# Kernel optimization log

Measured on AMD Instinct MI355X. Metric: run time of the kernel, lower is better.

Reference implementation:

```python
import jax, jax.numpy as jnp
import numpy as np

N = 524288
D_IN = 128


def setup_inputs() -> dict:
    key = jax.random.key(0)
    k_x, k_th, k_fb, k_xi, k_gb = jax.random.split(key, 5)
    X = jax.random.normal(k_x, (N, D_IN), dtype=jnp.float32)
    # f_linear: D_in -> H2 (=N); weight theta is [N, D_in], bias f_bias [N]
    theta = jax.random.normal(k_th, (N, D_IN), dtype=jnp.float32) * 0.02
    f_bias = jax.random.normal(k_fb, (N,), dtype=jnp.float32) * 0.02
    # g_linear: D_in -> H1 (=2); weight xi is [2, D_in], bias g_bias [2]
    xi = jax.random.normal(k_xi, (2, D_IN), dtype=jnp.float32) * 0.02
    g_bias = jax.random.normal(k_gb, (2,), dtype=jnp.float32) * 0.02
    return {"X": X, "theta": theta, "f_bias": f_bias, "xi": xi, "g_bias": g_bias}


def reference(X, theta, f_bias, xi, g_bias):
    # V[i] = relu(g_linear(X[i]))  -> one batched GEMM: [N,2]
    V = jax.nn.relu(X @ xi.T + g_bias)
    # Full W[i,j] = relu(X[i] . theta[j] + f_bias[j]) is masked by the chord
    # mask eye(N) + offsets (i + 2^k - 1) % N for k in {0,1} = offsets {0, 1}.
    # So only the diagonal and first (circulant) super-diagonal survive:
    # w_diag[i] = relu(X[i] . theta[i]       + f_bias[i])
    # w_sup[i]  = relu(X[i] . theta[(i+1)%N] + f_bias[(i+1)%N])
    w_diag = jax.nn.relu(jnp.einsum("nd,nd->n", X, theta) + f_bias)
    theta_next = jnp.roll(theta, -1, axis=0)
    f_bias_next = jnp.roll(f_bias, -1, axis=0)
    w_sup = jax.nn.relu(jnp.einsum("nd,nd->n", X, theta_next) + f_bias_next)
    # V0 = (W * chord_mask) @ V, computed sparsely: [N,2]
    V0 = w_diag[:, None] * V + w_sup[:, None] * jnp.roll(V, -1, axis=0)
    return V0
```

## Files before the change

### kernel.cpp

```cpp
#include <hip/hip_runtime.h>


constexpr int NROWS = 524288;
constexpr int D     = 128;

__device__ __forceinline__ float dot8(const float4& a, const float4& b,
                                      const float4& c, const float4& d) {
    return a.x*c.x + a.y*c.y + a.z*c.z + a.w*c.w
         + b.x*d.x + b.y*d.y + b.z*d.z + b.w*d.w;
}

__global__ __launch_bounds__(256, 4) void smf_kernel(
    const float* __restrict__ X,
    const float* __restrict__ theta,
    const float* __restrict__ f_bias,
    const float* __restrict__ xi,
    const float* __restrict__ g_bias,
    float* __restrict__ out)
{
    const int tid  = blockIdx.x * blockDim.x + threadIdx.x;
    const int wid  = tid >> 6;
    const int lane = threadIdx.x & 63;
    const int grp  = lane >> 4;
    const int q    = lane & 15;
    const int col  = q * 8;

    const int i   = wid * 4 + grp;
    const int ip1 = (i + 1 == NROWS) ? 0 : i + 1;

    const float* xrow  = X     + (size_t)i   * D + col;
    const float* xnrow = X     + (size_t)ip1 * D + col;
    const float* trow  = theta + (size_t)i   * D + col;
    const float* tnrow = theta + (size_t)ip1 * D + col;

    const float4 xa   = *reinterpret_cast<const float4*>(xrow);
    const float4 xb   = *reinterpret_cast<const float4*>(xrow + 4);
    const float4 xna  = *reinterpret_cast<const float4*>(xnrow);
    const float4 xnb  = *reinterpret_cast<const float4*>(xnrow + 4);
    const float4 ta   = *reinterpret_cast<const float4*>(trow);
    const float4 tb   = *reinterpret_cast<const float4*>(trow + 4);
    const float4 tna  = *reinterpret_cast<const float4*>(tnrow);
    const float4 tnb  = *reinterpret_cast<const float4*>(tnrow + 4);
    const float4 xi0a = *reinterpret_cast<const float4*>(xi + col);
    const float4 xi0b = *reinterpret_cast<const float4*>(xi + col + 4);
    const float4 xi1a = *reinterpret_cast<const float4*>(xi + D + col);
    const float4 xi1b = *reinterpret_cast<const float4*>(xi + D + col + 4);

    const float fb  = f_bias[i];
    const float fbn = f_bias[ip1];
    const float gb0 = g_bias[0];
    const float gb1 = g_bias[1];

    float d_diag = dot8(xa, xb, ta, tb);
    float d_sup  = dot8(xa, xb, tna, tnb);
    float vi0    = dot8(xa, xb, xi0a, xi0b);
    float vi1    = dot8(xa, xb, xi1a, xi1b);
    float vn0    = dot8(xna, xnb, xi0a, xi0b);
    float vn1    = dot8(xna, xnb, xi1a, xi1b);

    #pragma unroll
    for (int m = 8; m >= 1; m >>= 1) {
        d_diag += __shfl_xor(d_diag, m, 64);
        d_sup  += __shfl_xor(d_sup,  m, 64);
        vi0    += __shfl_xor(vi0,    m, 64);
        vi1    += __shfl_xor(vi1,    m, 64);
        vn0    += __shfl_xor(vn0,    m, 64);
        vn1    += __shfl_xor(vn1,    m, 64);
    }

    if (q == 0) {
        const float w_diag = fmaxf(d_diag + fb,  0.f);
        const float w_sup  = fmaxf(d_sup  + fbn, 0.f);
        const float v0 = fmaxf(vi0 + gb0, 0.f);
        const float v1 = fmaxf(vi1 + gb1, 0.f);
        const float u0 = fmaxf(vn0 + gb0, 0.f);
        const float u1 = fmaxf(vn1 + gb1, 0.f);
        float2 o;
        o.x = w_diag * v0 + w_sup * u0;
        o.y = w_diag * v1 + w_sup * u1;
        *reinterpret_cast<float2*>(out + (size_t)i * 2) = o;
    }
}

extern "C" void kernel_launch(void* const* d_in, const int* in_sizes, int n_in,
                              void* d_out, int out_size, void* d_ws, size_t ws_size,
                              hipStream_t stream) {
    const float* X      = (const float*)d_in[0];
    const float* theta  = (const float*)d_in[1];
    const float* f_bias = (const float*)d_in[2];
    const float* xi     = (const float*)d_in[3];
    const float* g_bias = (const float*)d_in[4];
    float* out = (float*)d_out;

    const int threads = 256;
    const int blocks  = NROWS / 16;
    smf_kernel<<<blocks, threads, 0, stream>>>(X, theta, f_bias, xi, g_bias, out);
}
```

Baseline: 508.8 us.

## Process eight row-quads per wavefront with double-buffered register prefetch

Each wavefront now handles eight groups of four rows instead of one. The next tile's X, theta and bias loads are issued before the current tile's dot products and reductions run, so memory latency overlaps compute, and the xi/g_bias loads are amortized across more rows. The grid shrinks eightfold and launch bounds drop to 3 waves per EU to allow the extra registers. The risk is lower occupancy and fewer blocks in flight, which can hurt a purely bandwidth-bound kernel.

After: 507.5 us. About the same (-0.3%).

```diff
diff --git a/kernel.cpp b/kernel.cpp
--- a/kernel.cpp
+++ b/kernel.cpp
@@ -3,6 +3,12 @@
 
 constexpr int NROWS = 524288;
 constexpr int D     = 128;
+constexpr int TPW   = 8;
+
+struct Tile {
+    float4 xa, xb, xna, xnb, ta, tb, tna, tnb;
+    float fb, fbn;
+};
 
 __device__ __forceinline__ float dot8(const float4& a, const float4& b,
                                       const float4& c, const float4& d) {
@@ -10,7 +16,63 @@
          + b.x*d.x + b.y*d.y + b.z*d.z + b.w*d.w;
 }
 
-__global__ __launch_bounds__(256, 4) void smf_kernel(
+__device__ __forceinline__ void load_tile(int i, int col,
+    const float* __restrict__ X, const float* __restrict__ theta,
+    const float* __restrict__ f_bias, Tile& t)
+{
+    const int ip1 = (i + 1 == NROWS) ? 0 : i + 1;
+    const float* xrow  = X     + (size_t)i   * D + col;
+    const float* xnrow = X     + (size_t)ip1 * D + col;
+    const float* trow  = theta + (size_t)i   * D + col;
+    const float* tnrow = theta + (size_t)ip1 * D + col;
+    t.xa  = *reinterpret_cast<const float4*>(xrow);
+    t.xb  = *reinterpret_cast<const float4*>(xrow + 4);
+    t.xna = *reinterpret_cast<const float4*>(xnrow);
+    t.xnb = *reinterpret_cast<const float4*>(xnrow + 4);
+    t.ta  = *reinterpret_cast<const float4*>(trow);
+    t.tb  = *reinterpret_cast<const float4*>(trow + 4);
+    t.tna = *reinterpret_cast<const float4*>(tnrow);
+    t.tnb = *reinterpret_cast<const float4*>(tnrow + 4);
+    t.fb  = f_bias[i];
+    t.fbn = f_bias[ip1];
+}
+
+__device__ __forceinline__ void compute_store(const Tile& t, int i, int q,
+    const float4& xi0a, const float4& xi0b, const float4& xi1a, const float4& xi1b,
+    float gb0, float gb1, float* __restrict__ out)
+{
+    float d_diag = dot8(t.xa,  t.xb,  t.ta,  t.tb);
+    float d_sup  = dot8(t.xa,  t.xb,  t.tna, t.tnb);
+    float vi0    = dot8(t.xa,  t.xb,  xi0a,  xi0b);
+    float vi1    = dot8(t.xa,  t.xb,  xi1a,  xi1b);
+    float vn0    = dot8(t.xna, t.xnb, xi0a,  xi0b);
+    float vn1    = dot8(t.xna, t.xnb, xi1a,  xi1b);
+
+    #pragma unroll
+    for (int m = 8; m >= 1; m >>= 1) {
+        d_diag += __shfl_xor(d_diag, m, 64);
+        d_sup  += __shfl_xor(d_sup,  m, 64);
+        vi0    += __shfl_xor(vi0,    m, 64);
+        vi1    += __shfl_xor(vi1,    m, 64);
+        vn0    += __shfl_xor(vn0,    m, 64);
+        vn1    += __shfl_xor(vn1,    m, 64);
+    }
+
+    if (q == 0) {
+        const float w_diag = fmaxf(d_diag + t.fb,  0.f);
+        const float w_sup  = fmaxf(d_sup  + t.fbn, 0.f);
+        const float v0 = fmaxf(vi0 + gb0, 0.f);
+        const float v1 = fmaxf(vi1 + gb1, 0.f);
+        const float u0 = fmaxf(vn0 + gb0, 0.f);
+        const float u1 = fmaxf(vn1 + gb1, 0.f);
+        float2 o;
+        o.x = w_diag * v0 + w_sup * u0;
+        o.y = w_diag * v1 + w_sup * u1;
+        *reinterpret_cast<float2*>(out + (size_t)i * 2) = o;
+    }
+}
+
+__global__ __launch_bounds__(256, 3) void smf_kernel(
     const float* __restrict__ X,
     const float* __restrict__ theta,
     const float* __restrict__ f_bias,
@@ -25,60 +87,25 @@
     const int q    = lane & 15;
     const int col  = q * 8;
 
-    const int i   = wid * 4 + grp;
-    const int ip1 = (i + 1 == NROWS) ? 0 : i + 1;
+    const int row0 = wid * (4 * TPW) + grp;
 
-    const float* xrow  = X     + (size_t)i   * D + col;
-    const float* xnrow = X     + (size_t)ip1 * D + col;
-    const float* trow  = theta + (size_t)i   * D + col;
-    const float* tnrow = theta + (size_t)ip1 * D + col;
-
-    const float4 xa   = *reinterpret_cast<const float4*>(xrow);
-    const float4 xb   = *reinterpret_cast<const float4*>(xrow + 4);
-    const float4 xna  = *reinterpret_cast<const float4*>(xnrow);
-    const float4 xnb  = *reinterpret_cast<const float4*>(xnrow + 4);
-    const float4 ta   = *reinterpret_cast<const float4*>(trow);
-    const float4 tb   = *reinterpret_cast<const float4*>(trow + 4);
-    const float4 tna  = *reinterpret_cast<const float4*>(tnrow);
-    const float4 tnb  = *reinterpret_cast<const float4*>(tnrow + 4);
     const float4 xi0a = *reinterpret_cast<const float4*>(xi + col);
     const float4 xi0b = *reinterpret_cast<const float4*>(xi + col + 4);
     const float4 xi1a = *reinterpret_cast<const float4*>(xi + D + col);
     const float4 xi1b = *reinterpret_cast<const float4*>(xi + D + col + 4);
-
-    const float fb  = f_bias[i];
-    const float fbn = f_bias[ip1];
     const float gb0 = g_bias[0];
     const float gb1 = g_bias[1];
 
-    float d_diag = dot8(xa, xb, ta, tb);
-    float d_sup  = dot8(xa, xb, tna, tnb);
-    float vi0    = dot8(xa, xb, xi0a, xi0b);
-    float vi1    = dot8(xa, xb, xi1a, xi1b);
-    float vn0    = dot8(xna, xnb, xi0a, xi0b);
-    float vn1    = dot8(xna, xnb, xi1a, xi1b);
+    Tile t0, t1;
+    load_tile(row0, col, X, theta, f_bias, t0);
 
     #pragma unroll
-    for (int m = 8; m >= 1; m >>= 1) {
-        d_diag += __shfl_xor(d_diag, m, 64);
-        d_sup  += __shfl_xor(d_sup,  m, 64);
-        vi0    += __shfl_xor(vi0,    m, 64);
-        vi1    += __shfl_xor(vi1,    m, 64);
-        vn0    += __shfl_xor(vn0,    m, 64);
-        vn1    += __shfl_xor(vn1,    m, 64);
-    }
-
-    if (q == 0) {
-        const float w_diag = fmaxf(d_diag + fb,  0.f);
-        const float w_sup  = fmaxf(d_sup  + fbn, 0.f);
-        const float v0 = fmaxf(vi0 + gb0, 0.f);
-        const float v1 = fmaxf(vi1 + gb1, 0.f);
-        const float u0 = fmaxf(vn0 + gb0, 0.f);
-        const float u1 = fmaxf(vn1 + gb1, 0.f);
-        float2 o;
-        o.x = w_diag * v0 + w_sup * u0;
-        o.y = w_diag * v1 + w_sup * u1;
-        *reinterpret_cast<float2*>(out + (size_t)i * 2) = o;
+    for (int t = 0; t < TPW; ++t) {
+        Tile& cur = (t & 1) ? t1 : t0;
+        Tile& nxt = (t & 1) ? t0 : t1;
+        if (t + 1 < TPW)
+            load_tile(row0 + (t + 1) * 4, col, X, theta, f_bias, nxt);
+        compute_store(cur, row0 + t * 4, q, xi0a, xi0b, xi1a, xi1b, gb0, gb1, out);
     }
 }
 
@@ -93,6 +120,6 @@
     float* out = (float*)d_out;
 
     const int threads = 256;
-    const int blocks  = NROWS / 16;
+    const int blocks  = NROWS / (4 * TPW * 4);
     smf_kernel<<<blocks, threads, 0, stream>>>(X, theta, f_bias, xi, g_bias, out);
 }
```
